# Kernel tuning notes

Measured on AMD Instinct MI355X. Metric: run time of the kernel, lower is better.

## Reference

```python
import jax, jax.numpy as jnp
import numpy as np

B, T1, T2, V, D, H = 1024, 256, 256, 32004, 50, 64


def _lstm_scan(x, h0, c0, Wih, Whh, b):
    """PyTorch-gate-order LSTM over time. x: [B,T,D]; returns hs, cs: [B,T,H]."""
    def step(carry, xt):
        h, c = carry
        g = xt @ Wih.T + h @ Whh.T + b  # [B, 4H], gate order i,f,g,o
        i, f, gg, o = jnp.split(g, 4, axis=-1)
        c = jax.nn.sigmoid(f) * c + jax.nn.sigmoid(i) * jnp.tanh(gg)
        h = jax.nn.sigmoid(o) * jnp.tanh(c)
        return (h, c), (h, c)
    _, (hs, cs) = jax.lax.scan(step, (h0, c0), jnp.swapaxes(x, 0, 1))
    return jnp.swapaxes(hs, 0, 1), jnp.swapaxes(cs, 0, 1)


def setup_inputs() -> dict:
    key = jax.random.key(0)
    ks = jax.random.split(key, 20)
    s = 1.0 / np.sqrt(H).astype(np.float32)
    inp = {
        "sentence1": jax.random.randint(ks[0], (B, T1), 0, V),
        "sentence2": jax.random.randint(ks[1], (B, T2), 0, V),
        "s1_len": jax.random.randint(ks[2], (B, 1, H), 0, T1),
        "s2_len": jax.random.randint(ks[3], (B, 1, H), 0, T2),
        "s1_s": jax.random.randint(ks[4], (B,), 0, 2),
        "s2_s": jax.random.randint(ks[5], (B,), 0, 2),
        "emb": jax.random.normal(ks[6], (V, D), jnp.float32),
        "Wih1": jax.random.uniform(ks[7], (4 * H, D), jnp.float32, -s, s),
        "Whh1": jax.random.uniform(ks[8], (4 * H, H), jnp.float32, -s, s),
        "bih1": jax.random.uniform(ks[9], (4 * H,), jnp.float32, -s, s),
        "bhh1": jax.random.uniform(ks[10], (4 * H,), jnp.float32, -s, s),
        "Wih2": jax.random.uniform(ks[11], (4 * H, D), jnp.float32, -s, s),
        "Whh2": jax.random.uniform(ks[12], (4 * H, H), jnp.float32, -s, s),
        "bih2": jax.random.uniform(ks[13], (4 * H,), jnp.float32, -s, s),
        "bhh2": jax.random.uniform(ks[14], (4 * H,), jnp.float32, -s, s),
        "Wl1": jax.random.uniform(ks[15], (128, H), jnp.float32, -s, s),
        "bl1": jax.random.uniform(ks[16], (128,), jnp.float32, -s, s),
        "Wl2": jax.random.uniform(ks[17], (4, 128), jnp.float32, -0.1, 0.1),
        "bl2": jax.random.uniform(ks[18], (4,), jnp.float32, -0.1, 0.1),
    }
    return inp


def reference(sentence1, sentence2, s1_len, s2_len, s1_s, s2_s, emb,
              Wih1, Whh1, bih1, bhh1, Wih2, Whh2, bih2, bhh2, Wl1, bl1, Wl2, bl2):
    embed1 = emb[sentence1]  # [B,T1,D]
    embed2 = emb[sentence2]  # [B,T2,D]
    h0 = jnp.zeros((B, H), embed1.dtype)
    c0 = jnp.zeros((B, H), embed1.dtype)
    # manual LSTMCell loop in original == scanned LSTM, keep all h,c per step
    h, c = _lstm_scan(embed1, h0, c0, Wih1, Whh1, bih1 + bhh1)  # [B,T1,H]
    gather_h = jnp.take_along_axis(h, s1_len, axis=1)[:, 0, :]  # [B,H]
    gather_c = jnp.take_along_axis(c, s1_len, axis=1)[:, 0, :]
    out, _ = _lstm_scan(embed2, gather_h, gather_c, Wih2, Whh2, bih2 + bhh2)
    out = jnp.take_along_axis(out, s2_len, axis=1)[:, 0, :]  # [B,H]
    out = jnp.tanh(out @ Wl1.T + bl1)  # dropout is identity at inference
    out = out @ Wl2.T + bl2  # [B,4]
    return out
```

## Files before the change

### kernel.cpp

```cpp
#include <hip/hip_runtime.h>

#define Bsz 1024
#define Tt  256
#define Vv  32004
#define Dd  50
#define Hh  64
#define MB  64

typedef __bf16 b16x8 __attribute__((ext_vector_type(8)));
typedef float  f32x4 __attribute__((ext_vector_type(4)));

__device__ __forceinline__ void barrier_novm() {
    asm volatile("s_waitcnt lgkmcnt(0)\n\ts_barrier" ::: "memory");
}
__device__ __forceinline__ float fexp2(float x) {
    float r;
    asm("v_exp_f32 %0, %1" : "=v"(r) : "v"(x));
    return r;
}
__device__ __forceinline__ float frcp(float x) {
    float r;
    asm("v_rcp_f32 %0, %1" : "=v"(r) : "v"(x));
    return r;
}
__device__ __forceinline__ float fsig(float x) {
    return frcp(1.0f + fexp2(x * -1.442695041f));
}
__device__ __forceinline__ float ftanh(float x) {
    return 2.0f * frcp(1.0f + fexp2(x * -2.885390082f)) - 1.0f;
}

__device__ __forceinline__ void cvt_hilo(const float* x, b16x8& hi, b16x8& lo) {
#pragma unroll
    for (int e = 0; e < 8; ++e) {
        const __bf16 h = (__bf16)x[e];
        hi[e] = h;
        lo[e] = (__bf16)(x[e] - (float)h);
    }
}

__launch_bounds__(256)
__global__ void build_tables(const float* __restrict__ emb,
                             const float* __restrict__ Wih1,
                             const float* __restrict__ bih1,
                             const float* __restrict__ bhh1,
                             const float* __restrict__ Wih2,
                             const float* __restrict__ bih2,
                             const float* __restrict__ bhh2,
                             float* __restrict__ tab1,
                             float* __restrict__ tab2) {
    const int tid  = threadIdx.x;
    const int w    = tid >> 6;
    const int lane = tid & 63;
    const int q    = lane >> 4;
    const int mn   = lane & 15;
    const int v0   = blockIdx.x * MB;

    const float* Wih = blockIdx.y ? Wih2 : Wih1;
    const float* bih = blockIdx.y ? bih2 : bih1;
    const float* bhh = blockIdx.y ? bhh2 : bhh1;
    float*       tab = blockIdx.y ? tab2 : tab1;

    b16x8 bh[4][2], bl[4][2];
    f32x4 bias4;
#pragma unroll
    for (int k = 0; k < 4; ++k) {
        const int g = 64 * k + 16 * w + mn;
        const float* wr = Wih + (size_t)g * Dd;
        float x[8];
#pragma unroll
        for (int j = 0; j < 8; j += 2) {
            const float2 t2 = *(const float2*)(wr + 8 * q + j);
            x[j] = t2.x; x[j + 1] = t2.y;
        }
        cvt_hilo(x, bh[k][0], bl[k][0]);
#pragma unroll
        for (int j = 0; j < 8; ++j) {
            const int col = 32 + 8 * q + j;
            x[j] = (col < Dd) ? wr[col] : 0.0f;
        }
        cvt_hilo(x, bh[k][1], bl[k][1]);
        bias4[k] = bih[g] + bhh[g];
    }

#pragma unroll
    for (int m = 0; m < 4; ++m) {
        const int v = v0 + 16 * m + mn;
        const float* er = emb + (size_t)(v < Vv ? v : Vv - 1) * Dd;
        b16x8 ah[2], al[2];
        float x[8];
#pragma unroll
        for (int j = 0; j < 8; j += 2) {
            const float2 t2 = *(const float2*)(er + 8 * q + j);
            x[j] = t2.x; x[j + 1] = t2.y;
        }
        cvt_hilo(x, ah[0], al[0]);
#pragma unroll
        for (int j = 0; j < 8; ++j) {
            const int col = 32 + 8 * q + j;
            x[j] = (col < Dd) ? er[col] : 0.0f;
        }
        cvt_hilo(x, ah[1], al[1]);

        f32x4 acc[4];
#pragma unroll
        for (int k = 0; k < 4; ++k) {
            f32x4 a = {0.0f, 0.0f, 0.0f, 0.0f};
#pragma unroll
            for (int kh = 0; kh < 2; ++kh) {
                a = __builtin_amdgcn_mfma_f32_16x16x32_bf16(ah[kh], bh[k][kh], a, 0, 0, 0);
                a = __builtin_amdgcn_mfma_f32_16x16x32_bf16(ah[kh], bl[k][kh], a, 0, 0, 0);
                a = __builtin_amdgcn_mfma_f32_16x16x32_bf16(al[kh], bh[k][kh], a, 0, 0, 0);
            }
            acc[k] = a;
        }
#pragma unroll
        for (int r = 0; r < 4; ++r) {
            const int vr = v0 + 16 * m + 4 * q + r;
            if (vr < Vv) {
                f32x4 o;
                o[0] = acc[0][r] + bias4[0];
                o[1] = acc[1][r] + bias4[1];
                o[2] = acc[2][r] + bias4[2];
                o[3] = acc[3][r] + bias4[3];
                *(f32x4*)(tab + (size_t)vr * 256 + (16 * w + mn) * 4) = o;
            }
        }
    }
}

__launch_bounds__(256, 1)
__global__ void lstm_main(const int*   __restrict__ s1,
                          const int*   __restrict__ s2,
                          const int*   __restrict__ len1,
                          const int*   __restrict__ len2,
                          const float* __restrict__ tab1,
                          const float* __restrict__ tab2,
                          const float* __restrict__ Whh1,
                          const float* __restrict__ Whh2,
                          const float* __restrict__ Wl1,
                          const float* __restrict__ bl1,
                          const float* __restrict__ Wl2,
                          const float* __restrict__ bl2,
                          float* __restrict__ out) {
    const int tid  = threadIdx.x;
    const int w    = tid >> 6;
    const int lane = tid & 63;
    const int q    = lane >> 4;
    const int mn   = lane & 15;
    const int row  = mn & 3;
    const bool sb0 = (mn >> 2) & 1;
    const bool sb1 = (mn >> 3) & 1;
    const int u_own = 16 * w + 4 * q + (mn >> 2);
    const int b0   = blockIdx.x * 4;

    __shared__ __align__(16) __bf16 hsh[2][4][96];
    __shared__ int   toklds[Tt][4];
    __shared__ float h2s[4][64];
    __shared__ float ys[4][128];

    float c = 0.0f, selh = 0.0f, selc = 0.0f;
    const f32x4 zero4 = {0.0f, 0.0f, 0.0f, 0.0f};

    for (int phase = 0; phase < 2; ++phase) {
        const float* tab  = phase ? tab2 : tab1;
        const float* Whh  = phase ? Whh2 : Whh1;
        const int*   sent = phase ? s2 : s1;
        const int*   lenp = phase ? len2 : len1;

        for (int i = tid; i < 4 * Tt; i += 256)
            toklds[i & 255][i >> 8] = sent[(size_t)(b0 + (i >> 8)) * Tt + (i & 255)];

        b16x8 af[8];
#pragma unroll
        for (int k = 0; k < 4; ++k) {
            const int gate = 64 * k + 16 * w + mn;
#pragma unroll
            for (int kh = 0; kh < 2; ++kh) {
                const float* ar = Whh + (size_t)gate * Hh + kh * 32 + q * 8;
                const float4 f0 = *(const float4*)ar;
                const float4 f1 = *(const float4*)(ar + 4);
                b16x8 a;
                a[0] = (__bf16)f0.x; a[1] = (__bf16)f0.y;
                a[2] = (__bf16)f0.z; a[3] = (__bf16)f0.w;
                a[4] = (__bf16)f1.x; a[5] = (__bf16)f1.y;
                a[6] = (__bf16)f1.z; a[7] = (__bf16)f1.w;
                af[2 * k + kh] = a;
            }
        }

        const int mi = lenp[(size_t)(b0 + row) * Hh + u_own];

        const float h0f = phase ? selh : 0.0f;
        c = phase ? selc : 0.0f;
        hsh[0][row][u_own] = (__bf16)h0f;
        selh = 0.0f; selc = 0.0f;
        __syncthreads();

        const float* tu = tab + 4 * u_own;
        f32x4 Sa, Sb, Sc, Sd;
        auto prime = [&](int t, f32x4& S) {
            S = *(const f32x4*)(tu + (size_t)toklds[t][row] * 256);
        };
        prime(0, Sa); prime(1, Sb); prime(2, Sc); prime(3, Sd);

        auto pick = [&](const f32x4& a) -> float {
            const float e01 = sb0 ? a[1] : a[0];
            const float e23 = sb0 ? a[3] : a[2];
            return sb1 ? e23 : e01;
        };

        auto step = [&](int t, f32x4& S, int rb, int wb) {
            const b16x8 bf0 = *(const b16x8*)&hsh[rb][row][q * 8];
            const b16x8 bf1 = *(const b16x8*)&hsh[rb][row][32 + q * 8];
            const int tnext = (t + 4 < Tt) ? t + 4 : Tt - 1;
            const int tk = toklds[tnext][row];

            f32x4 aG = __builtin_amdgcn_mfma_f32_16x16x32_bf16(af[4], bf0, zero4, 0, 0, 0);
            aG = __builtin_amdgcn_mfma_f32_16x16x32_bf16(af[5], bf1, aG, 0, 0, 0);
            f32x4 aI = __builtin_amdgcn_mfma_f32_16x16x32_bf16(af[0], bf0, zero4, 0, 0, 0);
            aI = __builtin_amdgcn_mfma_f32_16x16x32_bf16(af[1], bf1, aI, 0, 0, 0);
            f32x4 aF = __builtin_amdgcn_mfma_f32_16x16x32_bf16(af[2], bf0, zero4, 0, 0, 0);
            aF = __builtin_amdgcn_mfma_f32_16x16x32_bf16(af[3], bf1, aF, 0, 0, 0);
            f32x4 aO = __builtin_amdgcn_mfma_f32_16x16x32_bf16(af[6], bf0, zero4, 0, 0, 0);
            aO = __builtin_amdgcn_mfma_f32_16x16x32_bf16(af[7], bf1, aO, 0, 0, 0);

            const float gG = pick(aG) + S[2];
            const float gI = pick(aI) + S[0];
            const float gF = pick(aF) + S[1];
            const float gO = pick(aO) + S[3];
            S = *(const f32x4*)(tu + (size_t)tk * 256);

            const float gv = ftanh(gG);
            const float iv = fsig(gI);
            const float fv = fsig(gF);
            const float ov = fsig(gO);
            c = fv * c + iv * gv;
            const float hv = ov * ftanh(c);
            hsh[wb][row][u_own] = (__bf16)hv;
            if (t == mi) { selh = hv; selc = c; }
            barrier_novm();
        };

        for (int t = 0; t < Tt; t += 4) {
            step(t,     Sa, 0, 1);
            step(t + 1, Sb, 1, 0);
            step(t + 2, Sc, 0, 1);
            step(t + 3, Sd, 1, 0);
        }
    }

    h2s[row][u_own] = selh;
    __syncthreads();
#pragma unroll
    for (int p = 0; p < 2; ++p) {
        const int idx = tid + 256 * p;
        const int rr = idx >> 7, n = idx & 127;
        float a = bl1[n];
        const float* wl = Wl1 + n * 64;
#pragma unroll 8
        for (int k = 0; k < 64; ++k) a += h2s[rr][k] * wl[k];
        ys[rr][n] = ftanh(a);
    }
    __syncthreads();
    if (tid < 16) {
        const int rr = tid >> 2, o = tid & 3;
        float a = bl2[o];
        const float* wl = Wl2 + o * 128;
#pragma unroll 8
        for (int k = 0; k < 128; ++k) a += ys[rr][k] * wl[k];
        out[(size_t)(b0 + rr) * 4 + o] = a;
    }
}

extern "C" void kernel_launch(void* const* d_in, const int* in_sizes, int n_in,
                              void* d_out, int out_size, void* d_ws, size_t ws_size,
                              hipStream_t stream) {
    const int*   s1   = (const int*)d_in[0];
    const int*   s2   = (const int*)d_in[1];
    const int*   l1   = (const int*)d_in[2];
    const int*   l2   = (const int*)d_in[3];
    const float* emb  = (const float*)d_in[6];
    const float* Wih1 = (const float*)d_in[7];
    const float* Whh1 = (const float*)d_in[8];
    const float* bih1 = (const float*)d_in[9];
    const float* bhh1 = (const float*)d_in[10];
    const float* Wih2 = (const float*)d_in[11];
    const float* Whh2 = (const float*)d_in[12];
    const float* bih2 = (const float*)d_in[13];
    const float* bhh2 = (const float*)d_in[14];
    const float* Wl1  = (const float*)d_in[15];
    const float* bl1  = (const float*)d_in[16];
    const float* Wl2  = (const float*)d_in[17];
    const float* bl2  = (const float*)d_in[18];
    float* out = (float*)d_out;

    float* tab1 = (float*)d_ws;
    float* tab2 = tab1 + (size_t)Vv * 256;

    dim3 grid((Vv + MB - 1) / MB, 2);
    build_tables<<<grid, 256, 0, stream>>>(emb, Wih1, bih1, bhh1,
                                           Wih2, bih2, bhh2, tab1, tab2);
    lstm_main<<<Bsz / 4, 256, 0, stream>>>(s1, s2, l1, l2, tab1, tab2,
                                           Whh1, Whh2, Wl1, bl1, Wl2, bl2, out);
}
```

Baseline: 283.3 us.

## Stage table-building operands in LDS and break MFMA accumulation chains in recurrence

Result: slower. 306.9 us (+8.3%).

```diff
diff --git a/kernel.cpp b/kernel.cpp
--- a/kernel.cpp
+++ b/kernel.cpp
@@ -5,7 +5,7 @@
 #define Vv  32004
 #define Dd  50
 #define Hh  64
-#define MB  64
+#define MB  128
 
 typedef __bf16 b16x8 __attribute__((ext_vector_type(8)));
 typedef float  f32x4 __attribute__((ext_vector_type(4)));
@@ -61,44 +61,62 @@
     const float* bhh = blockIdx.y ? bhh2 : bhh1;
     float*       tab = blockIdx.y ? tab2 : tab1;
 
+    __shared__ __align__(16) float wlds[256 * Dd];
+    __shared__ __align__(16) float elds[MB * Dd];
+
+    for (int d4 = tid; d4 < 256 * Dd / 4; d4 += 256)
+        *(float4*)&wlds[4 * d4] = *(const float4*)(Wih + 4 * d4);
+    {
+        const int ebase = v0 * Dd;
+        const int elim  = Vv * Dd - ebase;
+        const int mx    = Vv * Dd - 1;
+        for (int d4 = tid; d4 < MB * Dd / 4; d4 += 256) {
+            const int d = 4 * d4;
+            float4 v;
+            if (d + 4 <= elim) {
+                v = *(const float4*)(emb + ebase + d);
+            } else {
+                v.x = emb[min(ebase + d,     mx)];
+                v.y = emb[min(ebase + d + 1, mx)];
+                v.z = emb[min(ebase + d + 2, mx)];
+                v.w = emb[min(ebase + d + 3, mx)];
+            }
+            *(float4*)&elds[d] = v;
+        }
+    }
+    __syncthreads();
+
     b16x8 bh[4][2], bl[4][2];
     f32x4 bias4;
 #pragma unroll
     for (int k = 0; k < 4; ++k) {
         const int g = 64 * k + 16 * w + mn;
-        const float* wr = Wih + (size_t)g * Dd;
+        const int base = g * Dd;
         float x[8];
 #pragma unroll
-        for (int j = 0; j < 8; j += 2) {
-            const float2 t2 = *(const float2*)(wr + 8 * q + j);
-            x[j] = t2.x; x[j + 1] = t2.y;
-        }
+        for (int j = 0; j < 8; ++j) x[j] = wlds[base + 8 * q + j];
         cvt_hilo(x, bh[k][0], bl[k][0]);
 #pragma unroll
         for (int j = 0; j < 8; ++j) {
             const int col = 32 + 8 * q + j;
-            x[j] = (col < Dd) ? wr[col] : 0.0f;
+            x[j] = (col < Dd) ? wlds[base + col] : 0.0f;
         }
         cvt_hilo(x, bh[k][1], bl[k][1]);
         bias4[k] = bih[g] + bhh[g];
     }
 
-#pragma unroll
-    for (int m = 0; m < 4; ++m) {
-        const int v = v0 + 16 * m + mn;
-        const float* er = emb + (size_t)(v < Vv ? v : Vv - 1) * Dd;
+#pragma unroll 1
+    for (int m = 0; m < MB / 16; ++m) {
+        const int base = (16 * m + mn) * Dd;
         b16x8 ah[2], al[2];
         float x[8];
 #pragma unroll
-        for (int j = 0; j < 8; j += 2) {
-            const float2 t2 = *(const float2*)(er + 8 * q + j);
-            x[j] = t2.x; x[j + 1] = t2.y;
-        }
+        for (int j = 0; j < 8; ++j) x[j] = elds[base + 8 * q + j];
         cvt_hilo(x, ah[0], al[0]);
 #pragma unroll
         for (int j = 0; j < 8; ++j) {
             const int col = 32 + 8 * q + j;
-            x[j] = (col < Dd) ? er[col] : 0.0f;
+            x[j] = (col < Dd) ? elds[base + col] : 0.0f;
         }
         cvt_hilo(x, ah[1], al[1]);
 
@@ -214,22 +232,22 @@
             const b16x8 bf0 = *(const b16x8*)&hsh[rb][row][q * 8];
             const b16x8 bf1 = *(const b16x8*)&hsh[rb][row][32 + q * 8];
             const int tnext = (t + 4 < Tt) ? t + 4 : Tt - 1;
-            const int tk = toklds[tnext][row];
-
-            f32x4 aG = __builtin_amdgcn_mfma_f32_16x16x32_bf16(af[4], bf0, zero4, 0, 0, 0);
-            aG = __builtin_amdgcn_mfma_f32_16x16x32_bf16(af[5], bf1, aG, 0, 0, 0);
-            f32x4 aI = __builtin_amdgcn_mfma_f32_16x16x32_bf16(af[0], bf0, zero4, 0, 0, 0);
-            aI = __builtin_amdgcn_mfma_f32_16x16x32_bf16(af[1], bf1, aI, 0, 0, 0);
-            f32x4 aF = __builtin_amdgcn_mfma_f32_16x16x32_bf16(af[2], bf0, zero4, 0, 0, 0);
-            aF = __builtin_amdgcn_mfma_f32_16x16x32_bf16(af[3], bf1, aF, 0, 0, 0);
-            f32x4 aO = __builtin_amdgcn_mfma_f32_16x16x32_bf16(af[6], bf0, zero4, 0, 0, 0);
-            aO = __builtin_amdgcn_mfma_f32_16x16x32_bf16(af[7], bf1, aO, 0, 0, 0);
-
-            const float gG = pick(aG) + S[2];
-            const float gI = pick(aI) + S[0];
-            const float gF = pick(aF) + S[1];
-            const float gO = pick(aO) + S[3];
-            S = *(const f32x4*)(tu + (size_t)tk * 256);
+            const f32x4 Snew = *(const f32x4*)(tu + (size_t)toklds[tnext][row] * 256);
+
+            f32x4 aG0 = __builtin_amdgcn_mfma_f32_16x16x32_bf16(af[4], bf0, zero4, 0, 0, 0);
+            f32x4 aG1 = __builtin_amdgcn_mfma_f32_16x16x32_bf16(af[5], bf1, zero4, 0, 0, 0);
+            f32x4 aI0 = __builtin_amdgcn_mfma_f32_16x16x32_bf16(af[0], bf0, zero4, 0, 0, 0);
+            f32x4 aI1 = __builtin_amdgcn_mfma_f32_16x16x32_bf16(af[1], bf1, zero4, 0, 0, 0);
+            f32x4 aF0 = __builtin_amdgcn_mfma_f32_16x16x32_bf16(af[2], bf0, zero4, 0, 0, 0);
+            f32x4 aF1 = __builtin_amdgcn_mfma_f32_16x16x32_bf16(af[3], bf1, zero4, 0, 0, 0);
+            f32x4 aO0 = __builtin_amdgcn_mfma_f32_16x16x32_bf16(af[6], bf0, zero4, 0, 0, 0);
+            f32x4 aO1 = __builtin_amdgcn_mfma_f32_16x16x32_bf16(af[7], bf1, zero4, 0, 0, 0);
+
+            const float gG = pick(aG0) + pick(aG1) + S[2];
+            const float gI = pick(aI0) + pick(aI1) + S[0];
+            const float gF = pick(aF0) + pick(aF1) + S[1];
+            const float gO = pick(aO0) + pick(aO1) + S[3];
+            S = Snew;
 
             const float gv = ftanh(gG);
             const float iv = fsig(gI);
```
